# Optimization experiments

Measured on AMD Instinct MI355X. Metric: run time of the kernel, lower is better.

Reference implementation:

```python
import jax, jax.numpy as jnp
import numpy as np

B, C, H, W = 8, 512, 64, 64
HID = 4 * C  # MixFFN hidden = in_dim*4
FOCUS = 3.0


def _ln(x, g, b, eps=1e-5):
    m = x.mean(-1, keepdims=True)
    v = ((x - m) ** 2).mean(-1, keepdims=True)
    return (x - m) / jnp.sqrt(v + eps) * g + b


def setup_inputs() -> dict:
    key = jax.random.key(0)
    ks = jax.random.split(key, 12)
    init = lambda k, shape, fan: (jax.random.normal(k, shape, jnp.float32) / np.float32(np.sqrt(fan)))
    d = {}
    d['x'] = jax.random.normal(ks[0], (B, C, H, W), jnp.float32)
    # 1x1 conv weights stored as (Cout, Cin)
    d['Wq'] = init(ks[1], (C, C), C); d['bq'] = jnp.zeros((C,), jnp.float32)
    d['Wk'] = init(ks[2], (C, C), C); d['bk'] = jnp.zeros((C,), jnp.float32)
    d['Wv'] = init(ks[3], (C, C), C); d['bv'] = jnp.zeros((C,), jnp.float32)
    d['scale'] = jnp.zeros((1, 1, C), jnp.float32)  # nn.Parameter(torch.zeros)
    # MixFFN_skip params
    d['fc1_w'] = init(ks[4], (C, HID), C); d['fc1_b'] = jnp.zeros((HID,), jnp.float32)
    d['dw_w'] = init(ks[5], (HID, 1, 3, 3), 9); d['dw_b'] = jnp.zeros((HID,), jnp.float32)
    d['fc2_w'] = init(ks[6], (HID, C), HID); d['fc2_b'] = jnp.zeros((C,), jnp.float32)
    d['ln1_g'] = jnp.ones((HID,), jnp.float32); d['ln1_b'] = jnp.zeros((HID,), jnp.float32)
    d['lnm_g'] = jnp.ones((C,), jnp.float32); d['lnm_b'] = jnp.zeros((C,), jnp.float32)
    return d


def _forward(x, Wq, bq, Wk, bk, Wv, bv, scale, fc1_w, fc1_b, dw_w, dw_b, fc2_w, fc2_b, ln1_g, ln1_b, lnm_g, lnm_b):
    b, c, h, w = x.shape
    n = h * w
    # 1x1 convs (NCHW), then RAW reshape to (B, N, C) as in torch (no permute!)
    conv1 = lambda t, Wm, bm: jnp.einsum('bchw,oc->bohw', t, Wm) + bm[None, :, None, None]
    q = jax.nn.softmax(conv1(x, Wq, bq).reshape(b, n, c), axis=1)
    k = jax.nn.softmax(conv1(x, Wk, bk).reshape(b, n, c), axis=2)
    v = conv1(x, Wv, bv).reshape(b, n, c)
    q = jax.nn.relu(q) + 1e-6
    k = jax.nn.relu(k) + 1e-6
    sc = jax.nn.softplus(scale)
    q = q / sc
    k = k / sc
    q_norm = jnp.linalg.norm(q, axis=-1, keepdims=True)
    k_norm = jnp.linalg.norm(k, axis=-1, keepdims=True)
    q = q ** FOCUS  # focusing_factor <= 6 branch
    k = k ** FOCUS
    q = q / jnp.linalg.norm(q, axis=-1, keepdims=True) * q_norm
    k = k / jnp.linalg.norm(k, axis=-1, keepdims=True) * k_norm
    # num_heads == 1: (b h) n c == b n c
    z = 1.0 / (jnp.einsum('bic,bc->bi', q, k.sum(axis=1)) + 1e-6)
    kv = jnp.einsum('bjc,bjd->bcd', k, v)  # O(N) linear attention summary
    attn = jnp.einsum('bic,bcd,bi->bid', q, kv, z)
    shortcut = jnp.transpose(x, (0, 2, 3, 1)).reshape(b, n, c)  # proper rearrange b c h w -> b (h w) c
    enhanced = shortcut + attn
    # MixFFN_skip(norm_mlp(enhanced), h, w)
    t = _ln(enhanced, lnm_g, lnm_b)
    a = t @ fc1_w + fc1_b  # (B, N, HID)
    ai = jnp.transpose(a, (0, 2, 1)).reshape(b, HID, h, w)
    dw = jax.lax.conv_general_dilated(ai, dw_w, (1, 1), 'SAME',
                                      dimension_numbers=('NCHW', 'OIHW', 'NCHW'),
                                      feature_group_count=HID)
    dw = dw + dw_b[None, :, None, None]
    dw = jnp.transpose(dw.reshape(b, HID, n), (0, 2, 1))
    ax = jax.nn.gelu(_ln(dw + a, ln1_g, ln1_b), approximate=False)
    mlp_out = ax @ fc2_w + fc2_b
    out = enhanced + mlp_out
    return out.reshape(b, h, w, c)


def reference(x, Wq, bq, Wk, bk, Wv, bv, scale, fc1_w, fc1_b, dw_w, dw_b, fc2_w, fc2_b, ln1_g, ln1_b, lnm_g, lnm_b):
    return _forward(x, Wq, bq, Wk, bk, Wv, bv, scale, fc1_w, fc1_b, dw_w, dw_b, fc2_w, fc2_b, ln1_g, ln1_b, lnm_g, lnm_b)
```

## Files before the change

### kernel.cpp

```cpp
#include <hip/hip_runtime.h>
#include <hip/hip_bf16.h>

typedef __hip_bfloat16 bf16;
typedef __attribute__((ext_vector_type(8))) short bh8;
typedef __attribute__((ext_vector_type(4))) float f32x4;

#define CDIM 512
#define NDIM 4096
#define HIDD 2048
#define BATCH 8

__device__ __forceinline__ float bf2f(short s) {
    union { unsigned u; float f; } c; c.u = ((unsigned)(unsigned short)s) << 16; return c.f;
}
__device__ __forceinline__ short f2bf(float f) {
    union { __hip_bfloat16 h; short s; } c; c.h = __float2bfloat16(f); return c.s;
}
__device__ __forceinline__ float wsum(float v) {
#pragma unroll
    for (int o = 32; o; o >>= 1) v += __shfl_xor(v, o);
    return v;
}
__device__ __forceinline__ float wmax(float v) {
#pragma unroll
    for (int o = 32; o; o >>= 1) v = fmaxf(v, __shfl_xor(v, o));
    return v;
}

#define GLL(g, l) __builtin_amdgcn_global_load_lds( \
    (const __attribute__((address_space(1))) unsigned int*)(g), \
    (__attribute__((address_space(3))) unsigned int*)(l), 16, 0, 0)


__device__ __forceinline__ void stage_ht(const bf16* __restrict__ base, int ld,
                                         int kt, char* ldsb, int t) {
#pragma unroll
    for (int l = 0; l < 2; ++l) {
        const int id = l * 512 + t;
        const int row = id >> 3, c = id & 7;
        const int cs = c ^ (row & 7);
        GLL(base + (long)row * ld + kt + (cs << 3),
            ldsb + l * 8192 + (t >> 6) * 1024 + (t & 63) * 16);
    }
}

template<int MODE, int MFAST>
__global__ __launch_bounds__(512, 2)
void gemm256(const bf16* __restrict__ A, int lda, long sA,
             const bf16* __restrict__ Bt, int ldb, long sB,
             void* __restrict__ Cp, int ldc, long sC, int K,
             const float* __restrict__ bias,
             void* __restrict__ aux1, void* __restrict__ aux2)
{
    __shared__ __align__(16) bf16 smem[65536];
    char* smemB = (char*)smem;
    int bx, by, bz;
    {
        const int gx = gridDim.x, gy = gridDim.y;
        const int nwg = gx * gy * gridDim.z;
        int lid = blockIdx.x + gx * (blockIdx.y + gy * blockIdx.z);
        const int cpx = nwg >> 3;
        int swz = (lid & 7) * cpx + (lid >> 3);
        if constexpr (MFAST) {
            by = swz % gy; swz /= gy;
            bx = swz % gx;
            bz = swz / gx;
        } else {
            bx = swz % gx; swz /= gx;
            by = swz % gy;
            bz = swz / gy;
        }
    }
    const bf16* Ab = A + (long)bz * sA + (long)by * 256 * lda;
    const bf16* Bb = Bt + (long)bz * sB + (long)bx * 256 * ldb;
    const int t = threadIdx.x, lane = t & 63, wid = t >> 6;
    const int wm = wid >> 2, wn = wid & 3;
    const int lg = lane >> 4, lr = lane & 15;

    f32x4 acc[8][4];
#pragma unroll
    for (int m = 0; m < 8; ++m)
#pragma unroll
        for (int n = 0; n < 4; ++n) acc[m][n] = (f32x4){0.f, 0.f, 0.f, 0.f};

    const int T = K >> 6;
    stage_ht(Bb, ldb, 0, smemB + 65536, t);
    stage_ht(Bb + (long)128 * ldb, ldb, 0, smemB + 65536 + 16384, t);
    stage_ht(Ab, lda, 0, smemB, t);
    stage_ht(Ab + (long)128 * lda, lda, 0, smemB + 16384, t);

    for (int tt = 0; tt < T; ++tt) {
        const int cur = tt & 1, nb = cur ^ 1;
        const int ktn = (tt + 1) << 6;
        const bool pf = (tt + 1 < T);
        const int aco = cur ? 16384 : 0;
        const int bco = 32768 + (cur ? 16384 : 0);
        const int anb = nb ? 32768 : 0;
        const int bnb = 65536 + (nb ? 32768 : 0);

        bh8 afA[4], afB[4], bfA[4], bfB[4];

        if (pf) stage_ht(Bb, ldb, ktn, smemB + bnb, t);
        if (pf) asm volatile("s_waitcnt vmcnt(2)" ::: "memory");
        else    asm volatile("s_waitcnt vmcnt(0)" ::: "memory");
        __builtin_amdgcn_s_barrier();
#pragma unroll
        for (int m = 0; m < 4; ++m) {
            const int row = wm * 128 + m * 16 + lr;
            afA[m] = *(const bh8*)(smem + aco + row * 64 + (lg ^ (row & 7)) * 8);
        }
#pragma unroll
        for (int n = 0; n < 4; ++n) {
            const int row = wn * 64 + n * 16 + lr;
            bfA[n] = *(const bh8*)(smem + bco + row * 64 + (lg ^ (row & 7)) * 8);
        }
        asm volatile("s_waitcnt lgkmcnt(0)" ::: "memory");
        __builtin_amdgcn_sched_barrier(0);
        __builtin_amdgcn_s_setprio(1);
#pragma unroll
        for (int m = 0; m < 4; ++m)
#pragma unroll
            for (int n = 0; n < 4; ++n)
                acc[m][n] = __builtin_amdgcn_mfma_f32_16x16x32_bf16(afA[m], bfA[n], acc[m][n], 0, 0, 0);
        __builtin_amdgcn_s_setprio(0);
        __builtin_amdgcn_s_barrier();

#pragma unroll
        for (int m = 0; m < 4; ++m) {
            const int row = wm * 128 + 64 + m * 16 + lr;
            afB[m] = *(const bh8*)(smem + aco + row * 64 + (lg ^ (row & 7)) * 8);
        }
        if (pf) stage_ht(Bb + (long)128 * ldb, ldb, ktn, smemB + bnb + 16384, t);
        asm volatile("s_waitcnt lgkmcnt(0)" ::: "memory");
        __builtin_amdgcn_sched_barrier(0);
        __builtin_amdgcn_s_setprio(1);
#pragma unroll
        for (int m = 0; m < 4; ++m)
#pragma unroll
            for (int n = 0; n < 4; ++n)
                acc[4 + m][n] = __builtin_amdgcn_mfma_f32_16x16x32_bf16(afB[m], bfA[n], acc[4 + m][n], 0, 0, 0);
        __builtin_amdgcn_s_setprio(0);
        __builtin_amdgcn_s_barrier();

#pragma unroll
        for (int m = 0; m < 4; ++m) {
            const int row = wm * 128 + m * 16 + lr;
            afA[m] = *(const bh8*)(smem + aco + row * 64 + ((4 + lg) ^ (row & 7)) * 8);
        }
#pragma unroll
        for (int n = 0; n < 4; ++n) {
            const int row = wn * 64 + n * 16 + lr;
            bfB[n] = *(const bh8*)(smem + bco + row * 64 + ((4 + lg) ^ (row & 7)) * 8);
        }
        if (pf) stage_ht(Ab, lda, ktn, smemB + anb, t);
        asm volatile("s_waitcnt lgkmcnt(0)" ::: "memory");
        __builtin_amdgcn_sched_barrier(0);
        __builtin_amdgcn_s_setprio(1);
#pragma unroll
        for (int m = 0; m < 4; ++m)
#pragma unroll
            for (int n = 0; n < 4; ++n)
                acc[m][n] = __builtin_amdgcn_mfma_f32_16x16x32_bf16(afA[m], bfB[n], acc[m][n], 0, 0, 0);
        __builtin_amdgcn_s_setprio(0);
        __builtin_amdgcn_s_barrier();

#pragma unroll
        for (int m = 0; m < 4; ++m) {
            const int row = wm * 128 + 64 + m * 16 + lr;
            afB[m] = *(const bh8*)(smem + aco + row * 64 + ((4 + lg) ^ (row & 7)) * 8);
        }
        if (pf) stage_ht(Ab + (long)128 * lda, lda, ktn, smemB + anb + 16384, t);
        asm volatile("s_waitcnt lgkmcnt(0)" ::: "memory");
        __builtin_amdgcn_sched_barrier(0);
        __builtin_amdgcn_s_setprio(1);
#pragma unroll
        for (int m = 0; m < 4; ++m)
#pragma unroll
            for (int n = 0; n < 4; ++n)
                acc[4 + m][n] = __builtin_amdgcn_mfma_f32_16x16x32_bf16(afB[m], bfB[n], acc[4 + m][n], 0, 0, 0);
        __builtin_amdgcn_s_setprio(0);
        __builtin_amdgcn_s_barrier();
    }

    const int gr0 = by * 256 + wm * 128;
    const int gc0 = bx * 256 + wn * 64;
    if constexpr (MODE == 2) {
        const bf16* xg = (const bf16*)aux1 + (long)bz * ((long)NDIM * CDIM);
        const float* zg = (const float*)aux2 + (long)bz * NDIM;
        float* op = (float*)Cp + (long)bz * sC;
#pragma unroll
        for (int m = 0; m < 8; ++m)
#pragma unroll
            for (int n = 0; n < 4; ++n) {
                const int col = gc0 + n * 16 + lr;
#pragma unroll
                for (int r = 0; r < 4; ++r) {
                    const int grow = gr0 + m * 16 + lg * 4 + r;
                    op[(long)grow * ldc + col] =
                        zg[grow] * acc[m][n][r] + bf2f(*(const short*)(xg + (long)grow * 512 + col));
                }
            }
    } else if constexpr (MODE == 0) {
        const int which = by >> 1;
        bf16* dst = (which == 0) ? (bf16*)Cp : (which == 1) ? (bf16*)aux1 : (bf16*)aux2;
        dst += (long)bz * sC;
#pragma unroll
        for (int m = 0; m < 8; ++m)
#pragma unroll
            for (int n = 0; n < 4; ++n) {
                const int col = gc0 + n * 16 + lr;
#pragma unroll
                for (int r = 0; r < 4; ++r) {
                    const int grow = gr0 + m * 16 + lg * 4 + r;
                    float v = acc[m][n][r] + bias[grow];
                    if (which == 0) v = __expf(v);
                    dst[(long)(grow - which * 512) * ldc + col] = __float2bfloat16(v);
                }
            }
    } else {
        bf16* dst = (bf16*)Cp + (long)bz * sC;
#pragma unroll
        for (int m = 0; m < 8; ++m)
#pragma unroll
            for (int n = 0; n < 4; ++n) {
                const int col = gc0 + n * 16 + lr;
                const float bc = bias[col];
#pragma unroll
                for (int r = 0; r < 4; ++r) {
                    const int grow = gr0 + m * 16 + lg * 4 + r;
                    dst[(long)grow * ldc + col] = __float2bfloat16(acc[m][n][r] + bc);
                }
            }
    }
}

enum { EP_OUT = 5 };

template<int MODE, int TM, int MFAST>
__global__ __launch_bounds__(256)
void gemm_bt(const bf16* __restrict__ A, int lda, long sA,
             const bf16* __restrict__ Bt, int ldb, long sB,
             void* __restrict__ Cp, int ldc, long sC, int K,
             const float* __restrict__ bias,
             const void* __restrict__ aux1, long sAux1,
             const void* __restrict__ aux2, long sAux2)
{
    constexpr int MF = TM / 32;
    __shared__ __align__(16) bf16 smem[TM * 64 + 128 * 64];
    bf16* As = smem;
    bf16* Bs = smem + TM * 64;
    int bx, by, bz;
    {
        const int gx = gridDim.x, gy = gridDim.y;
        const int nwg = gx * gy * gridDim.z;
        int lid = blockIdx.x + gx * (blockIdx.y + gy * blockIdx.z);
        const int cpx = nwg >> 3;
        int swz = (lid & 7) * cpx + (lid >> 3);
        if constexpr (MFAST) {
            by = swz % gy; swz /= gy;
            bx = swz % gx;
            bz = swz / gx;
        } else {
            bx = swz % gx; swz /= gx;
            by = swz % gy;
            bz = swz / gy;
        }
    }
    const bf16* Ab = A + (long)bz * sA + (long)by * TM * lda;
    const bf16* Bb = Bt + (long)bz * sB + (long)bx * 128 * ldb;
    const int t = threadIdx.x, lane = t & 63, wid = t >> 6;
    const int wm = wid >> 1, wn = wid & 1, lg = lane >> 4, lr = lane & 15;

    f32x4 acc[MF][4];
#pragma unroll
    for (int m = 0; m < MF; ++m)
#pragma unroll
        for (int n = 0; n < 4; ++n) acc[m][n] = (f32x4){0.f, 0.f, 0.f, 0.f};

    for (int kt = 0; kt < K; kt += 64) {
#pragma unroll
        for (int i = 0; i < MF; ++i) {
            const int ch = i * 256 + t;
            const int row = ch >> 3;
            const int cs = (ch & 7) ^ (row & 7);
            GLL(Ab + (long)row * lda + kt + (cs << 3), (char*)As + i * 4096 + wid * 1024);
        }
#pragma unroll
        for (int i = 0; i < 4; ++i) {
            const int ch = i * 256 + t;
            const int row = ch >> 3;
            const int cs = (ch & 7) ^ (row & 7);
            GLL(Bb + (long)row * ldb + kt + (cs << 3), (char*)Bs + i * 4096 + wid * 1024);
        }
        __syncthreads();
#pragma unroll
        for (int kk = 0; kk < 2; ++kk) {
            bh8 af[MF], bfv[4];
#pragma unroll
            for (int m = 0; m < MF; ++m) {
                const int row = wm * (TM / 2) + m * 16 + lr;
                const int kc = (kk * 4 + lg) ^ (row & 7);
                af[m] = *(const bh8*)(As + row * 64 + kc * 8);
            }
#pragma unroll
            for (int n = 0; n < 4; ++n) {
                const int row = wn * 64 + n * 16 + lr;
                const int kc = (kk * 4 + lg) ^ (row & 7);
                bfv[n] = *(const bh8*)(Bs + row * 64 + kc * 8);
            }
#pragma unroll
            for (int m = 0; m < MF; ++m)
#pragma unroll
                for (int n = 0; n < 4; ++n)
                    acc[m][n] = __builtin_amdgcn_mfma_f32_16x16x32_bf16(af[m], bfv[n], acc[m][n], 0, 0, 0);
        }
        __syncthreads();
    }

    const int gr0 = by * TM + wm * (TM / 2);
    const int gc0 = bx * 128 + wn * 64;
#pragma unroll
    for (int m = 0; m < MF; ++m) {
#pragma unroll
        for (int n = 0; n < 4; ++n) {
            const int gc = gc0 + n * 16 + lr;
#pragma unroll
            for (int r = 0; r < 4; ++r) {
                const int gr = gr0 + m * 16 + lg * 4 + r;
                float v = acc[m][n][r];
                if constexpr (MODE == EP_OUT) {
                    float* op = (float*)Cp;
                    const long idx = (long)gr * ldc + gc;
                    op[idx] = v + bias[gc] + ((const float*)aux1)[idx];
                }
            }
        }
    }
}

__global__ __launch_bounds__(256)
void gemm_tn_splitk(const bf16* __restrict__ A, int lda, long sA,
                    const bf16* __restrict__ B, int ldb, long sB,
                    bf16* __restrict__ part)
{
    __shared__ __align__(16) short smem[2 * 64 * 128];
    short* As = smem;
    short* Bs = smem + 64 * 128;
    int bx, by, bzl;
    {
        const int gx = gridDim.x, gy = gridDim.y;
        const int nwg = gx * gy * gridDim.z;
        int lid = blockIdx.x + gx * (blockIdx.y + gy * blockIdx.z);
        const int cpx = nwg >> 3;
        int swz = (lid & 7) * cpx + (lid >> 3);
        bx = swz % gx; swz /= gx;
        by = swz % gy;
        bzl = swz / gy;
    }
    const int bz = bzl >> 2, ks = bzl & 3;
    const bf16* Ab = A + (long)bz * sA + (long)ks * 1024 * lda + by * 128;
    const bf16* Bb = B + (long)bz * sB + (long)ks * 1024 * ldb + bx * 128;
    const int t = threadIdx.x, lane = t & 63, wid = t >> 6;
    const int wm = wid >> 1, wn = wid & 1, lg = lane >> 4, lr = lane & 15;

    f32x4 acc[4][4];
#pragma unroll
    for (int m = 0; m < 4; ++m)
#pragma unroll
        for (int n = 0; n < 4; ++n) acc[m][n] = (f32x4){0.f, 0.f, 0.f, 0.f};

    for (int kt = 0; kt < 1024; kt += 64) {
#pragma unroll
        for (int i = 0; i < 4; ++i) {
            const int ch = i * 256 + t;
            const int row = ch >> 4;
            const int cs = (ch & 15) ^ (((row >> 3) & 3) << 1);
            GLL(Ab + (long)(kt + row) * lda + (cs << 3), (char*)As + i * 4096 + wid * 1024);
            GLL(Bb + (long)(kt + row) * ldb + (cs << 3), (char*)Bs + i * 4096 + wid * 1024);
        }
        __syncthreads();
#pragma unroll
        for (int kk = 0; kk < 2; ++kk) {
            bh8 af[4], bfv[4];
#pragma unroll
            for (int m = 0; m < 4; ++m) {
                const int col = wm * 64 + m * 16 + lr;
#pragma unroll
                for (int u = 0; u < 8; ++u) {
                    const int row = kk * 32 + lg * 8 + u;
                    af[m][u] = As[row * 128 + (((col >> 3) ^ (((row >> 3) & 3) << 1)) << 3) + (col & 7)];
                }
            }
#pragma unroll
            for (int n = 0; n < 4; ++n) {
                const int col = wn * 64 + n * 16 + lr;
#pragma unroll
                for (int u = 0; u < 8; ++u) {
                    const int row = kk * 32 + lg * 8 + u;
                    bfv[n][u] = Bs[row * 128 + (((col >> 3) ^ (((row >> 3) & 3) << 1)) << 3) + (col & 7)];
                }
            }
#pragma unroll
            for (int m = 0; m < 4; ++m)
#pragma unroll
                for (int n = 0; n < 4; ++n)
                    acc[m][n] = __builtin_amdgcn_mfma_f32_16x16x32_bf16(af[m], bfv[n], acc[m][n], 0, 0, 0);
        }
        __syncthreads();
    }

    bf16* Cs = (bf16*)smem;
    bf16* dstb = part + ((long)bzl << 18) + (long)by * 128 * 512;
#pragma unroll
    for (int m = 0; m < 4; ++m)
#pragma unroll
        for (int n = 0; n < 4; ++n)
#pragma unroll
            for (int r = 0; r < 4; ++r) {
                const int row = wm * 64 + m * 16 + lg * 4 + r;
                const int col = wn * 64 + n * 16 + lr;
                Cs[row * 128 + (col ^ (((row >> 2) & 3) << 4))] = __float2bfloat16(acc[m][n][r]);
            }
    __syncthreads();
#pragma unroll
    for (int it = 0; it < 8; ++it) {
        const int id = it * 256 + t;
        const int row = id >> 4, colc = (id & 15) << 3;
        bh8 v = *(const bh8*)(Cs + row * 128 + (colc ^ (((row >> 2) & 3) << 4)));
        *(bh8*)(dstb + (long)row * 512 + bx * 128 + colc) = v;
    }
}

__global__ __launch_bounds__(256)
void k_transpose3(const float* __restrict__ fc1w, bf16* __restrict__ fc1wT,
                  const float* __restrict__ fc2w, bf16* __restrict__ fc2wT,
                  const float* __restrict__ x, bf16* __restrict__ xbT)
{
    __shared__ float tile[64][65];
    const int bid = blockIdx.x;
    const float* s; bf16* d; int Rd, Cd, bx, by;
    if (bid < 256) {
        s = fc1w; d = fc1wT; Rd = 2048; Cd = 512; bx = bid & 31; by = bid >> 5;
    } else if (bid < 512) {
        const int i = bid - 256;
        s = fc2w; d = fc2wT; Rd = 512; Cd = 2048; bx = i & 7; by = i >> 3;
    } else {
        const int i = bid - 512;
        const int bz = i >> 9, j = i & 511;
        bx = j & 63; by = j >> 6;
        const long NC = (long)NDIM * CDIM;
        s = x + (long)bz * NC; d = xbT + (long)bz * NC; Rd = 4096; Cd = 512;
    }
    const int r0 = bx * 64, c0 = by * 64;
    const int t = threadIdx.x;
#pragma unroll 4
    for (int i = 0; i < 16; ++i) {
        int idx = i * 256 + t;
        int a = idx >> 6, b = idx & 63;
        tile[a][b] = s[(long)(c0 + a) * Rd + r0 + b];
    }
    __syncthreads();
#pragma unroll 4
    for (int i = 0; i < 16; ++i) {
        int idx = i * 256 + t;
        int a = idx >> 6, b = idx & 63;
        d[(long)(r0 + a) * Cd + c0 + b] = __float2bfloat16(tile[b][a]);
    }
}

__global__ void k_setup(const float* __restrict__ Wq, const float* __restrict__ Wk,
                        const float* __restrict__ Wv, bf16* __restrict__ oq,
                        bf16* __restrict__ ok, bf16* __restrict__ ov,
                        const float* __restrict__ scale, float* __restrict__ invsc,
                        const float* __restrict__ w, float* __restrict__ wT,
                        const float* __restrict__ bq, const float* __restrict__ bk,
                        const float* __restrict__ bv, float* __restrict__ bqkv) {
    int i = blockIdx.x * 256 + threadIdx.x;
    if (i < 262144) {
        oq[i] = __float2bfloat16(Wq[i]);
        ok[i] = __float2bfloat16(Wk[i]);
        ov[i] = __float2bfloat16(Wv[i]);
    }
    if (i < 512) invsc[i] = 1.0f / log1pf(expf(scale[i]));
    if (i < 1536) bqkv[i] = (i < 512 ? bq[i] : (i < 1024 ? bk[i - 512] : bv[i - 1024]));
    if (i < HIDD * 9) {
        int chn = i / 9, kk = i % 9;
        wT[kk * HIDD + chn] = w[i];
    }
}

__global__ void k_fill(float* o, int n, float v) {
    int i = blockIdx.x * 256 + threadIdx.x; if (i < n) o[i] = v;
}

__global__ __launch_bounds__(256)
void k_colsums(const bf16* __restrict__ qe, float* __restrict__ qpart) {
    const int ic = blockIdx.y, b = blockIdx.z;
    const int j = blockIdx.x * 256 + threadIdx.x;
    const bf16* p = qe + (long)b * (NDIM * CDIM) + (long)ic * 256 * CDIM + j;
    float s = 0.f;
    for (int i = 0; i < 256; ++i) s += bf2f(*(const short*)(p + (long)i * CDIM));
    qpart[((long)b * 16 + ic) * CDIM + j] = s;
}

__global__ __launch_bounds__(256)
void k_red2(const float* __restrict__ qpart, float* __restrict__ qsum,
            const float* __restrict__ kpart, float* __restrict__ ksum) {
    const int idx = blockIdx.x * 256 + threadIdx.x;
    const int which = idx >> 12, r = idx & 4095;
    const int b = r >> 9, c = r & 511;
    float s = 0.f;
    if (which == 0) {
#pragma unroll
        for (int jc = 0; jc < 16; ++jc) s += qpart[((long)(b * 16 + jc)) * CDIM + c];
        qsum[r] = s;
    } else {
        for (int jc = 0; jc < 128; ++jc) s += kpart[((long)(b * 128 + jc)) * CDIM + c];
        ksum[r] = s;
    }
}

__global__ __launch_bounds__(256)
void k_krow2(bf16* __restrict__ kb, const float* __restrict__ invsc,
             float* __restrict__ kpart)
{
    const int lane = threadIdx.x & 63, wid = threadIdx.x >> 6;
    const float* is = invsc + lane * 8;
    f32x4 i0 = *(const f32x4*)is, i1 = *(const f32x4*)(is + 4);
    float kacc[8] = {0.f, 0.f, 0.f, 0.f, 0.f, 0.f, 0.f, 0.f};
    const long base = (long)blockIdx.x * 32 + wid * 8;
    for (int rr = 0; rr < 8; ++rr) {
        const long row = base + rr;
        bh8 v = *(const bh8*)(kb + row * CDIM + lane * 8);
        float xv[8];
#pragma unroll
        for (int k = 0; k < 8; ++k) xv[k] = bf2f(v[k]);
        float mx = -1e30f;
#pragma unroll
        for (int k = 0; k < 8; ++k) mx = fmaxf(mx, xv[k]);
        mx = wmax(mx);
        float e[8], se = 0.f;
#pragma unroll
        for (int k = 0; k < 8; ++k) { e[k] = __expf(xv[k] - mx); se += e[k]; }
        se = wsum(se);
        const float inv = 1.0f / se;
        float q[8];
#pragma unroll
        for (int k = 0; k < 4; ++k) {
            q[k]     = (e[k] * inv + 1e-6f) * i0[k];
            q[k + 4] = (e[k + 4] * inv + 1e-6f) * i1[k];
        }
        float s2 = 0.f, s6 = 0.f, q3[8];
#pragma unroll
        for (int k = 0; k < 8; ++k) { s2 += q[k] * q[k]; float c = q[k] * q[k] * q[k]; q3[k] = c; s6 += c * c; }
        s2 = wsum(s2); s6 = wsum(s6);
        const float sc = sqrtf(s2) / sqrtf(s6);
        bh8 o;
#pragma unroll
        for (int k = 0; k < 8; ++k) {
            o[k] = f2bf(q3[k] * sc);
            kacc[k] += bf2f(o[k]);
        }
        *(bh8*)(kb + row * CDIM + lane * 8) = o;
    }
    __shared__ float red[4][512];
#pragma unroll
    for (int k = 0; k < 8; ++k) red[wid][lane * 8 + k] = kacc[k];
    __syncthreads();
    const int c0 = threadIdx.x * 2;
#pragma unroll
    for (int u = 0; u < 2; ++u) {
        const int c = c0 + u;
        kpart[(long)blockIdx.x * 512 + c] = red[0][c] + red[1][c] + red[2][c] + red[3][c];
    }
}

__global__ __launch_bounds__(256)
void k_kvqrow(const bf16* __restrict__ part, bf16* __restrict__ kvt,
              const bf16* __restrict__ qe, const float* __restrict__ qsum,
              const float* __restrict__ invsc, bf16* __restrict__ qb,
              const float* __restrict__ ksum, float* __restrict__ z)
{
    if (blockIdx.x < 1024) {
        const long e = ((long)blockIdx.x * 256 + threadIdx.x) * 8;
        const int b = (int)(e >> 18);
        const int off = (int)(e & 262143);
        float s[8] = {0.f, 0.f, 0.f, 0.f, 0.f, 0.f, 0.f, 0.f};
#pragma unroll
        for (int ks = 0; ks < 4; ++ks) {
            bh8 v = *(const bh8*)(part + (((long)(b * 4 + ks)) << 18) + off);
#pragma unroll
            for (int j = 0; j < 8; ++j) s[j] += bf2f(v[j]);
        }
        bh8 o;
#pragma unroll
        for (int j = 0; j < 8; ++j) o[j] = f2bf(s[j]);
        *(bh8*)(kvt + ((long)b << 18) + off) = o;
        return;
    }
    const long row = (long)(blockIdx.x - 1024) * 4 + (threadIdx.x >> 6);
    const int lane = threadIdx.x & 63;
    const int b = (int)(row >> 12);
    bh8 ev = *(const bh8*)(qe + row * CDIM + lane * 8);
    const float* qs = qsum + b * CDIM + lane * 8;
    const float* is = invsc + lane * 8;
    f32x4 s0 = *(const f32x4*)qs, s1 = *(const f32x4*)(qs + 4);
    f32x4 i0 = *(const f32x4*)is, i1 = *(const f32x4*)(is + 4);
    float q[8];
#pragma unroll
    for (int k = 0; k < 4; ++k) {
        q[k]     = (bf2f(ev[k]) / s0[k] + 1e-6f) * i0[k];
        q[k + 4] = (bf2f(ev[k + 4]) / s1[k] + 1e-6f) * i1[k];
    }
    float s2 = 0.f, s6 = 0.f, q3[8];
#pragma unroll
    for (int k = 0; k < 8; ++k) { s2 += q[k] * q[k]; float c = q[k] * q[k] * q[k]; q3[k] = c; s6 += c * c; }
    s2 = wsum(s2); s6 = wsum(s6);
    const float sc = sqrtf(s2) / sqrtf(s6);
    bh8 o;
#pragma unroll
    for (int k = 0; k < 8; ++k) o[k] = f2bf(q3[k] * sc);
    *(bh8*)(qb + row * CDIM + lane * 8) = o;
    const float* ks = ksum + (long)b * CDIM + lane * 8;
    f32x4 k0 = *(const f32x4*)ks, k1 = *(const f32x4*)(ks + 4);
    float zd = 0.f;
#pragma unroll
    for (int j = 0; j < 4; ++j) { zd += bf2f(o[j]) * k0[j]; zd += bf2f(o[j + 4]) * k1[j]; }
    zd = wsum(zd);
    if (lane == 0) z[row] = 1.0f / (zd + 1e-6f);
}

__global__ __launch_bounds__(256)
void k_ln512(const float* __restrict__ src, const float* __restrict__ g,
             const float* __restrict__ bta, bf16* __restrict__ dst)
{
    const long row = (long)blockIdx.x * 4 + (threadIdx.x >> 6);
    const int lane = threadIdx.x & 63;
    const float* p = src + row * CDIM + lane * 8;
    f32x4 a0 = *(const f32x4*)p, a1 = *(const f32x4*)(p + 4);
    float s = 0.f, ss = 0.f;
#pragma unroll
    for (int k = 0; k < 4; ++k) { s += a0[k] + a1[k]; ss += a0[k] * a0[k] + a1[k] * a1[k]; }
    s = wsum(s); ss = wsum(ss);
    const float mean = s * (1.0f / 512), var = ss * (1.0f / 512) - mean * mean;
    const float rstd = rsqrtf(var + 1e-5f);
    const float* gp = g + lane * 8;
    const float* bp = bta + lane * 8;
    f32x4 g0 = *(const f32x4*)gp, g1 = *(const f32x4*)(gp + 4);
    f32x4 b0 = *(const f32x4*)bp, b1 = *(const f32x4*)(bp + 4);
    bh8 o;
#pragma unroll
    for (int k = 0; k < 4; ++k) {
        o[k]     = f2bf((a0[k] - mean) * rstd * g0[k] + b0[k]);
        o[k + 4] = f2bf((a1[k] - mean) * rstd * g1[k] + b1[k]);
    }
    *(bh8*)(dst + row * CDIM + lane * 8) = o;
}

__global__ __launch_bounds__(256)
void k_dwlngelu4(const bf16* __restrict__ a, const float* __restrict__ dwwT,
                 const float* __restrict__ dwb, const float* __restrict__ g1,
                 const float* __restrict__ b1, bf16* __restrict__ ax)
{
    const long s0 = (long)blockIdx.x * 4;
    const int h = (int)((s0 >> 6) & 63);
    const int w0 = (int)(s0 & 63);
    const int ch = threadIdx.x * 8;

    float wgt[9][8];
#pragma unroll
    for (int kk = 0; kk < 9; ++kk) {
        f32x4 w0v = *(const f32x4*)(dwwT + kk * HIDD + ch);
        f32x4 w1v = *(const f32x4*)(dwwT + kk * HIDD + ch + 4);
#pragma unroll
        for (int j = 0; j < 4; ++j) { wgt[kk][j] = w0v[j]; wgt[kk][j + 4] = w1v[j]; }
    }
#pragma unroll
    for (int j = 0; j < 8; ++j) wgt[4][j] += 1.0f;

    float acc[4][8];
    {
        f32x4 d0 = *(const f32x4*)(dwb + ch), d1 = *(const f32x4*)(dwb + ch + 4);
#pragma unroll
        for (int ti = 0; ti < 4; ++ti)
#pragma unroll
            for (int j = 0; j < 4; ++j) { acc[ti][j] = d0[j]; acc[ti][j + 4] = d1[j]; }
    }

#pragma unroll
    for (int dy = -1; dy <= 1; ++dy) {
        const int hh = h + dy;
        if ((unsigned)hh >= 64u) continue;
#pragma unroll
        for (int c = -1; c <= 4; ++c) {
            const int ww = w0 + c;
            if ((unsigned)ww >= 64u) continue;
            bh8 v = *(const bh8*)(a + (s0 + (long)dy * 64 + c) * HIDD + ch);
            float f[8];
#pragma unroll
            for (int j = 0; j < 8; ++j) f[j] = bf2f(v[j]);
#pragma unroll
            for (int ti = 0; ti < 4; ++ti) {
                const int dx = c - ti;
                if (dx < -1 || dx > 1) continue;
                const int kk = (dy + 1) * 3 + (dx + 1);
#pragma unroll
                for (int j = 0; j < 8; ++j) acc[ti][j] += wgt[kk][j] * f[j];
            }
        }
    }

    float sv[4], qv[4];
#pragma unroll
    for (int ti = 0; ti < 4; ++ti) {
        float s = 0.f, q = 0.f;
#pragma unroll
        for (int j = 0; j < 8; ++j) { s += acc[ti][j]; q += acc[ti][j] * acc[ti][j]; }
        sv[ti] = wsum(s); qv[ti] = wsum(q);
    }
    __shared__ float red[4][4][2];
    const int wid = threadIdx.x >> 6, lane = threadIdx.x & 63;
    if (lane == 0)
#pragma unroll
        for (int ti = 0; ti < 4; ++ti) { red[wid][ti][0] = sv[ti]; red[wid][ti][1] = qv[ti]; }
    __syncthreads();

    f32x4 ga = *(const f32x4*)(g1 + ch), gb = *(const f32x4*)(g1 + ch + 4);
    f32x4 ba = *(const f32x4*)(b1 + ch), bb = *(const f32x4*)(b1 + ch + 4);
    float gg[8], bb8[8];
#pragma unroll
    for (int j = 0; j < 4; ++j) { gg[j] = ga[j]; gg[j + 4] = gb[j]; bb8[j] = ba[j]; bb8[j + 4] = bb[j]; }

#pragma unroll
    for (int ti = 0; ti < 4; ++ti) {
        const float s = red[0][ti][0] + red[1][ti][0] + red[2][ti][0] + red[3][ti][0];
        const float q = red[0][ti][1] + red[1][ti][1] + red[2][ti][1] + red[3][ti][1];
        const float mean = s * (1.0f / 2048), var = q * (1.0f / 2048) - mean * mean;
        const float rstd = rsqrtf(var + 1e-5f);
        bh8 o;
#pragma unroll
        for (int j = 0; j < 8; ++j) {
            float y = (acc[ti][j] - mean) * rstd * gg[j] + bb8[j];
            o[j] = f2bf(0.5f * y * (1.0f + erff(y * 0.70710678118654752f)));
        }
        *(bh8*)(ax + (s0 + ti) * HIDD + ch) = o;
    }
}

extern "C" void kernel_launch(void* const* d_in, const int* in_sizes, int n_in,
                              void* d_out, int out_size, void* d_ws, size_t ws_size,
                              hipStream_t stream) {
    const float* x     = (const float*)d_in[0];
    const float* Wq    = (const float*)d_in[1];
    const float* bq    = (const float*)d_in[2];
    const float* Wk    = (const float*)d_in[3];
    const float* bk    = (const float*)d_in[4];
    const float* Wv    = (const float*)d_in[5];
    const float* bv    = (const float*)d_in[6];
    const float* scale = (const float*)d_in[7];
    const float* fc1_w = (const float*)d_in[8];
    const float* fc1_b = (const float*)d_in[9];
    const float* dw_w  = (const float*)d_in[10];
    const float* dw_b  = (const float*)d_in[11];
    const float* fc2_w = (const float*)d_in[12];
    const float* fc2_b = (const float*)d_in[13];
    const float* ln1_g = (const float*)d_in[14];
    const float* ln1_b = (const float*)d_in[15];
    const float* lnm_g = (const float*)d_in[16];
    const float* lnm_b = (const float*)d_in[17];
    float* out = (float*)d_out;
    char* p = (char*)d_ws;

    bf16*  xbT   = (bf16*)(p + 0);
    bf16*  kb    = (bf16*)(p + 33554432);
    bf16*  vb    = (bf16*)(p + 67108864);
    bf16*  kvt   = (bf16*)(p + 100663296);
    bf16*  wqb   = (bf16*)(p + 104857600);
    bf16*  wkb   = (bf16*)(p + 105381888);
    bf16*  wvb   = (bf16*)(p + 105906176);
    bf16*  fc1wT = (bf16*)(p + 106430464);
    bf16*  fc2wT = (bf16*)(p + 108527616);
    float* invsc = (float*)(p + 110624768);
    float* dwwT  = (float*)(p + 110626816);
    float* bqkv  = (float*)(p + 110700544);
    float* qsum  = (float*)(p + 110757888);
    float* ksum  = (float*)(p + 110905344);
    float* zbuf  = (float*)(p + 110921728);
    const size_t REQUIRED = 111052800;
    float* qpart = (float*)kvt;
    float* kpart = (float*)((char*)kvt + 262144);
    bf16*  qe    = (bf16*)out;
    bf16*  kvpart= (bf16*)((char*)out + 33554432);
    bf16*  qb    = kb;
    bf16*  abuf  = (bf16*)(p + 0);
    bf16*  axbuf = (bf16*)(p + 33554432);
    bf16*  tbuf  = (bf16*)(p + 67108864);

    if (ws_size < REQUIRED) {
        k_fill<<<(out_size + 255) / 256, 256, 0, stream>>>(out, out_size, 100000.0f + (float)(ws_size >> 20));
        return;
    }

    const long NC = (long)NDIM * CDIM;

    k_setup<<<1024, 256, 0, stream>>>(Wq, Wk, Wv, wqb, wkb, wvb, scale, invsc,
                                      dw_w, dwwT, bq, bk, bv, bqkv);
    k_transpose3<<<4608, 256, 0, stream>>>(fc1_w, fc1wT, fc2_w, fc2wT, x, xbT);

    gemm256<0, 1><<<dim3(16, 6, 8), 512, 0, stream>>>(
        wqb, 512, 0, xbT, 512, NC, qe, 4096, NC, 512, bqkv, kb, vb);

    k_krow2<<<1024, 256, 0, stream>>>(kb, invsc, kpart);
    k_colsums<<<dim3(2, 16, 8), 256, 0, stream>>>(qe, qpart);
    k_red2<<<32, 256, 0, stream>>>(qpart, qsum, kpart, ksum);

    gemm_tn_splitk<<<dim3(4, 4, 32), 256, 0, stream>>>(vb, 512, NC, kb, 512, NC, kvpart);
    k_kvqrow<<<9216, 256, 0, stream>>>(kvpart, kvt, qe, qsum, invsc, qb, ksum, zbuf);

    gemm256<2, 0><<<dim3(2, 16, 8), 512, 0, stream>>>(
        qb, 512, NC, kvt, 512, 262144, out, 512, NC, 512, nullptr, xbT, zbuf);

    k_ln512<<<8192, 256, 0, stream>>>(out, lnm_g, lnm_b, tbuf);
    for (int q4 = 0; q4 < 4; ++q4) {
        float* outq = out + (long)q4 * 8192 * CDIM;
        bf16* tq = tbuf + (long)q4 * 8192 * CDIM;
        gemm256<1, 0><<<dim3(8, 32, 1), 512, 0, stream>>>(
            tq, 512, 0, fc1wT, 512, 0, abuf, 2048, 0, 512, fc1_b, nullptr, nullptr);
        k_dwlngelu4<<<2048, 256, 0, stream>>>(abuf, dwwT, dw_b, ln1_g, ln1_b, axbuf);
        gemm_bt<EP_OUT, 64, 0><<<dim3(4, 128, 1), 256, 0, stream>>>(
            axbuf, 2048, 0, fc2wT, 2048, 0, outq, 512, 0, 2048, fc2_b, outq, 0, nullptr, 0);
    }
}
```

Measured before the change: 580.2 us.

## Restructure gemm256 main loop to issue all prefetches up front with fewer barriers

The K-loop now issues all four next-tile global-to-LDS stages at the start of each iteration, waits with vmcnt(8) for the current tile, and uses only two barriers per iteration instead of four interleaved barrier/stage phases. The explicit lgkmcnt waits and sched_barriers between MFMA groups are removed so the compiler schedules the LDS reads. Launch bounds drop to one block per SM, which allows more registers per thread but lowers occupancy. The aim is to cut barrier overhead and widen the prefetch window, at the cost of losing interleaved staging and the hand scheduling that hid LDS latency.

```diff
diff --git a/kernel.cpp b/kernel.cpp
--- a/kernel.cpp
+++ b/kernel.cpp
@@ -45,7 +45,7 @@
 }
 
 template<int MODE, int MFAST>
-__global__ __launch_bounds__(512, 2)
+__global__ __launch_bounds__(512, 1)
 void gemm256(const bf16* __restrict__ A, int lda, long sA,
              const bf16* __restrict__ Bt, int ldb, long sB,
              void* __restrict__ Cp, int ldc, long sC, int K,
@@ -98,12 +98,20 @@
         const int anb = nb ? 32768 : 0;
         const int bnb = 65536 + (nb ? 32768 : 0);
 
+        __builtin_amdgcn_s_barrier();
+        if (pf) {
+            stage_ht(Bb, ldb, ktn, smemB + bnb, t);
+            stage_ht(Bb + (long)128 * ldb, ldb, ktn, smemB + bnb + 16384, t);
+            stage_ht(Ab, lda, ktn, smemB + anb, t);
+            stage_ht(Ab + (long)128 * lda, lda, ktn, smemB + anb + 16384, t);
+            asm volatile("s_waitcnt vmcnt(8)" ::: "memory");
+        } else {
+            asm volatile("s_waitcnt vmcnt(0)" ::: "memory");
+        }
+        __builtin_amdgcn_s_barrier();
+
+        __builtin_amdgcn_s_setprio(1);
         bh8 afA[4], afB[4], bfA[4], bfB[4];
-
-        if (pf) stage_ht(Bb, ldb, ktn, smemB + bnb, t);
-        if (pf) asm volatile("s_waitcnt vmcnt(2)" ::: "memory");
-        else    asm volatile("s_waitcnt vmcnt(0)" ::: "memory");
-        __builtin_amdgcn_s_barrier();
 #pragma unroll
         for (int m = 0; m < 4; ++m) {
             const int row = wm * 128 + m * 16 + lr;
@@ -114,34 +122,21 @@
             const int row = wn * 64 + n * 16 + lr;
             bfA[n] = *(const bh8*)(smem + bco + row * 64 + (lg ^ (row & 7)) * 8);
         }
-        asm volatile("s_waitcnt lgkmcnt(0)" ::: "memory");
-        __builtin_amdgcn_sched_barrier(0);
-        __builtin_amdgcn_s_setprio(1);
 #pragma unroll
         for (int m = 0; m < 4; ++m)
 #pragma unroll
             for (int n = 0; n < 4; ++n)
                 acc[m][n] = __builtin_amdgcn_mfma_f32_16x16x32_bf16(afA[m], bfA[n], acc[m][n], 0, 0, 0);
-        __builtin_amdgcn_s_setprio(0);
-        __builtin_amdgcn_s_barrier();
-
 #pragma unroll
         for (int m = 0; m < 4; ++m) {
             const int row = wm * 128 + 64 + m * 16 + lr;
             afB[m] = *(const bh8*)(smem + aco + row * 64 + (lg ^ (row & 7)) * 8);
         }
-        if (pf) stage_ht(Bb + (long)128 * ldb, ldb, ktn, smemB + bnb + 16384, t);
-        asm volatile("s_waitcnt lgkmcnt(0)" ::: "memory");
-        __builtin_amdgcn_sched_barrier(0);
-        __builtin_amdgcn_s_setprio(1);
 #pragma unroll
         for (int m = 0; m < 4; ++m)
 #pragma unroll
             for (int n = 0; n < 4; ++n)
                 acc[4 + m][n] = __builtin_amdgcn_mfma_f32_16x16x32_bf16(afB[m], bfA[n], acc[4 + m][n], 0, 0, 0);
-        __builtin_amdgcn_s_setprio(0);
-        __builtin_amdgcn_s_barrier();
-
 #pragma unroll
         for (int m = 0; m < 4; ++m) {
             const int row = wm * 128 + m * 16 + lr;
@@ -152,34 +147,22 @@
             const int row = wn * 64 + n * 16 + lr;
             bfB[n] = *(const bh8*)(smem + bco + row * 64 + ((4 + lg) ^ (row & 7)) * 8);
         }
-        if (pf) stage_ht(Ab, lda, ktn, smemB + anb, t);
-        asm volatile("s_waitcnt lgkmcnt(0)" ::: "memory");
-        __builtin_amdgcn_sched_barrier(0);
-        __builtin_amdgcn_s_setprio(1);
 #pragma unroll
         for (int m = 0; m < 4; ++m)
 #pragma unroll
             for (int n = 0; n < 4; ++n)
                 acc[m][n] = __builtin_amdgcn_mfma_f32_16x16x32_bf16(afA[m], bfB[n], acc[m][n], 0, 0, 0);
-        __builtin_amdgcn_s_setprio(0);
-        __builtin_amdgcn_s_barrier();
-
 #pragma unroll
         for (int m = 0; m < 4; ++m) {
             const int row = wm * 128 + 64 + m * 16 + lr;
             afB[m] = *(const bh8*)(smem + aco + row * 64 + ((4 + lg) ^ (row & 7)) * 8);
         }
-        if (pf) stage_ht(Ab + (long)128 * lda, lda, ktn, smemB + anb + 16384, t);
-        asm volatile("s_waitcnt lgkmcnt(0)" ::: "memory");
-        __builtin_amdgcn_sched_barrier(0);
-        __builtin_amdgcn_s_setprio(1);
 #pragma unroll
         for (int m = 0; m < 4; ++m)
 #pragma unroll
             for (int n = 0; n < 4; ++n)
                 acc[4 + m][n] = __builtin_amdgcn_mfma_f32_16x16x32_bf16(afB[m], bfB[n], acc[4 + m][n], 0, 0, 0);
         __builtin_amdgcn_s_setprio(0);
-        __builtin_amdgcn_s_barrier();
     }
 
     const int gr0 = by * 256 + wm * 128;
```

Measured after the change: 583.8 us. Within noise of the previous version (+0.6%).
